# Kernel optimization log

Hardware: AMD Instinct MI355X
Metric: run time of the kernel (lower is better)

The kernel has to match this reference:

```python
import jax, jax.numpy as jnp
import numpy as np
import math

WIN = 2
TOPK = 3
GH, GW = 4, 4  # gabor splatting grid == upsampled window size


def _window_partition(img, ws):
    # img: (B, C, H, W) -> (B, num_windows, ws*ws, C)
    B, C, H, W = img.shape
    x = img.transpose(0, 2, 3, 1)  # B,H,W,C
    x = x.reshape(B, H // ws, ws, W // ws, ws, C)
    x = x.transpose(0, 1, 3, 2, 4, 5).reshape(B, -1, ws * ws, C)
    return x


def _gabor_map(theta, sigma, lam, psi, gamma):
    # build num 4x4 Gabor kernels from per-component params -> (num, GH, GW)
    cy = jnp.arange(GH, dtype=jnp.float32) - (GH - 1) / 2.0
    cx = jnp.arange(GW, dtype=jnp.float32) - (GW - 1) / 2.0
    yy, xx = jnp.meshgrid(cy, cx, indexing='ij')  # (GH, GW)
    th = theta[:, None, None] * (2.0 * jnp.pi)
    xp = xx[None] * jnp.cos(th) + yy[None] * jnp.sin(th)
    yp = -xx[None] * jnp.sin(th) + yy[None] * jnp.cos(th)
    sig = sigma[:, None, None] + 0.5  # keep positive
    lmb = lam[:, None, None] + 0.5
    gam = gamma[:, None, None]
    env = jnp.exp(-(xp ** 2 + (gam ** 2) * yp ** 2) / (2.0 * sig ** 2))
    carrier = jnp.cos(2.0 * jnp.pi * xp / lmb + psi[:, None, None])
    return env * carrier  # (num, GH, GW)


def setup_inputs() -> dict:
    key = jax.random.key(0)
    ks = jax.random.split(key, 8)
    B, Nt, Ns, C = 64, 64, 4096, 256
    return {
        'z': jax.random.normal(ks[0], (B, Nt, C), dtype=jnp.float32),
        'x': jax.random.normal(ks[1], (B, Ns, C), dtype=jnp.float32),
        'gabor_theta': jax.random.uniform(ks[2], (16,), dtype=jnp.float32),
        'gabor_sigma': jax.random.uniform(ks[3], (16,), dtype=jnp.float32),
        'gabor_lam': jax.random.uniform(ks[4], (16,), dtype=jnp.float32),
        'gabor_psi': jax.random.uniform(ks[5], (16,), dtype=jnp.float32),
        'gabor_gamma': jax.random.uniform(ks[6], (16,), dtype=jnp.float32),
        'gabor_weight': jax.random.normal(ks[7], (16,), dtype=jnp.float32),
    }


def reference(z, x, gabor_theta, gabor_sigma, gabor_lam, gabor_psi,
              gabor_gamma, gabor_weight):
    B, Nt, C = z.shape
    ht = int(math.isqrt(Nt))
    _, Ns, _ = x.shape
    hs = int(math.isqrt(Ns))

    z_img = z.transpose(0, 2, 1).reshape(B, C, ht, ht)
    z_max = z_img.max(axis=(2, 3))  # AdaptiveMaxPool2d((1,1)) -> (B, C)

    x_img = x.transpose(0, 2, 1).reshape(B, C, hs, hs)
    x_windows = _window_partition(x_img, WIN)

    # grouped 1x1 xcorr == per-pixel dot product with template vector
    response = jnp.einsum('bchw,bc->bhw', x_img, z_max)[:, None]  # (B,1,hs,hs)
    r_windows = _window_partition(response, WIN)
    win_mean = r_windows.mean(axis=2)[..., 0]  # (B, nW)

    _, idx = jax.lax.top_k(win_mean, TOPK)  # (B, TOPK)
    x_sel = jnp.take_along_axis(x_windows, idx[:, :, None, None], axis=1)
    x_win = x_sel.reshape(B, TOPK, WIN, WIN, C).transpose(0, 1, 4, 2, 3)
    x_win = x_win.reshape(B * TOPK, C, WIN, WIN)

    x_up = jax.image.resize(x_win, (B * TOPK, C, GH, GW), method='bilinear')

    g = _gabor_map(gabor_theta, gabor_sigma, gabor_lam, gabor_psi, gabor_gamma)
    gmap = jnp.einsum('k,khw->hw', gabor_weight, g)  # (GH, GW)
    splat = x_up * gmap  # gabor splatting as multiplicative spatial modulation

    res = (splat + x_up).reshape(B, TOPK, C, GH * GW)
    res = res.transpose(0, 1, 3, 2).reshape(B, TOPK * GH * GW, C)
    return res
```

## Files before the change

### kernel.cpp

```cpp
#include <hip/hip_runtime.h>
#include <math.h>

#define TWO_PI 6.28318530717958647692f

typedef float vfloat4 __attribute__((ext_vector_type(4)));


__global__ void k_zmax(const float* __restrict__ z, float* __restrict__ zmax) {
    int b = blockIdx.x;
    int c = threadIdx.x;
    const float* zp = z + (size_t)b * 64 * 256 + c;
    float m = -INFINITY;
#pragma unroll
    for (int n = 0; n < 64; ++n) m = fmaxf(m, zp[n * 256]);
    zmax[b * 256 + c] = m;
}

__global__ void k_wmean(const float* __restrict__ x, const float* __restrict__ zmax,
                        float* __restrict__ wmean) {
    int blk  = blockIdx.x;
    int b    = blk >> 5;
    int wh   = blk & 31;
    int wave = threadIdx.x >> 6;
    int lane = threadIdx.x & 63;
    int g    = lane >> 4;
    int q    = lane & 15;

    const vfloat4* zm4 = (const vfloat4*)(zmax + b * 256);
    vfloat4 zm0 = zm4[q];
    vfloat4 zm1 = zm4[q + 16];
    vfloat4 zm2 = zm4[q + 32];
    vfloat4 zm3 = zm4[q + 48];

    const vfloat4* xb = (const vfloat4*)(x + (size_t)b * 4096 * 256);
    int trow = (2 * wh + (g >> 1)) * 64;
    float* wout = wmean + b * 1024 + wh * 32;

#pragma unroll
    for (int p = 0; p < 8; ++p) {
        int ww  = p * 4 + wave;
        int tok = trow + 2 * ww + (g & 1);
        const vfloat4* tp = xb + (size_t)tok * 64;
        vfloat4 v0 = __builtin_nontemporal_load(tp + q);
        vfloat4 v1 = __builtin_nontemporal_load(tp + q + 16);
        vfloat4 v2 = __builtin_nontemporal_load(tp + q + 32);
        vfloat4 v3 = __builtin_nontemporal_load(tp + q + 48);
        float d = v0.x * zm0.x + v0.y * zm0.y + v0.z * zm0.z + v0.w * zm0.w
                + v1.x * zm1.x + v1.y * zm1.y + v1.z * zm1.z + v1.w * zm1.w
                + v2.x * zm2.x + v2.y * zm2.y + v2.z * zm2.z + v2.w * zm2.w
                + v3.x * zm3.x + v3.y * zm3.y + v3.z * zm3.z + v3.w * zm3.w;
        d += __shfl_xor(d, 1, 64);
        d += __shfl_xor(d, 2, 64);
        d += __shfl_xor(d, 4, 64);
        d += __shfl_xor(d, 8, 64);
        d += __shfl_xor(d, 16, 64);
        d += __shfl_xor(d, 32, 64);
        if (lane == 0) wout[ww] = d * 0.25f;
    }
}

__global__ void k_out(const float* __restrict__ x, const float* __restrict__ wmean_g,
                      const float* __restrict__ theta, const float* __restrict__ sigma,
                      const float* __restrict__ lam,   const float* __restrict__ psi,
                      const float* __restrict__ gamma, const float* __restrict__ wgt,
                      float* __restrict__ out) {
    __shared__ float wmean[1024];
    __shared__ float rv[256];
    __shared__ int   ri[256];
    __shared__ float Xs[4 * 256];
    __shared__ float gm[16];
    __shared__ int   widx_s;

    int b = blockIdx.x / 3;
    int k = blockIdx.x % 3;
    int tid  = threadIdx.x;
    int tok  = tid >> 6;
    int lane = tid & 63;

    if (tid < 16) {
        int p = tid;
        float yy = (float)(p >> 2) - 1.5f;
        float xx = (float)(p & 3) - 1.5f;
        float acc = 0.0f;
        for (int kk = 0; kk < 16; ++kk) {
            float th = theta[kk] * TWO_PI;
            float sn, cs;
            sincosf(th, &sn, &cs);
            float xp = xx * cs + yy * sn;
            float yp = -xx * sn + yy * cs;
            float sig = sigma[kk] + 0.5f;
            float lmb = lam[kk] + 0.5f;
            float gam = gamma[kk];
            float env = expf(-(xp * xp + gam * gam * yp * yp) / (2.0f * sig * sig));
            float car = cosf(TWO_PI * xp / lmb + psi[kk]);
            acc += wgt[kk] * env * car;
        }
        gm[p] = 1.0f + acc;
    }

    for (int w = tid; w < 1024; w += 256) wmean[w] = wmean_g[b * 1024 + w];
    __syncthreads();

    for (int kk = 0; kk <= k; ++kk) {
        float bv = -INFINITY;
        int   bi = 1 << 30;
        for (int w = tid; w < 1024; w += 256) {
            float v = wmean[w];
            if (v > bv || (v == bv && w < bi)) { bv = v; bi = w; }
        }
        rv[tid] = bv; ri[tid] = bi;
        __syncthreads();
        for (int s = 128; s > 0; s >>= 1) {
            if (tid < s) {
                float v2 = rv[tid + s]; int i2 = ri[tid + s];
                if (v2 > rv[tid] || (v2 == rv[tid] && i2 < ri[tid])) { rv[tid] = v2; ri[tid] = i2; }
            }
            __syncthreads();
        }
        if (tid == 0) {
            widx_s = ri[0];
            wmean[ri[0]] = -INFINITY;
        }
        __syncthreads();
    }

    int widx = widx_s;
    int h0 = (widx >> 5) << 1;
    int w0 = (widx & 31) << 1;
    int token_id = (h0 + (tok >> 1)) * 64 + w0 + (tok & 1);
    float4 v = ((const float4*)(x + ((size_t)b * 4096 + token_id) * 256))[lane];
    ((float4*)Xs)[tok * 64 + lane] = v;
    __syncthreads();

    const float WT[4] = {1.0f, 0.75f, 0.25f, 0.0f};
    float4 x00 = ((const float4*)Xs)[0 * 64 + lane];
    float4 x01 = ((const float4*)Xs)[1 * 64 + lane];
    float4 x10 = ((const float4*)Xs)[2 * 64 + lane];
    float4 x11 = ((const float4*)Xs)[3 * 64 + lane];
    float4* ob = (float4*)(out + ((size_t)b * 48 + k * 16) * 256);
#pragma unroll
    for (int it = 0; it < 4; ++it) {
        int p  = it * 4 + (tid >> 6);
        int gy = p >> 2, gx = p & 3;
        float wy0 = WT[gy], wy1 = 1.0f - wy0;
        float wx0 = WT[gx], wx1 = 1.0f - wx0;
        float g = gm[p];
        float4 r;
        r.x = g * (wy0 * (wx0 * x00.x + wx1 * x01.x) + wy1 * (wx0 * x10.x + wx1 * x11.x));
        r.y = g * (wy0 * (wx0 * x00.y + wx1 * x01.y) + wy1 * (wx0 * x10.y + wx1 * x11.y));
        r.z = g * (wy0 * (wx0 * x00.z + wx1 * x01.z) + wy1 * (wx0 * x10.z + wx1 * x11.z));
        r.w = g * (wy0 * (wx0 * x00.w + wx1 * x01.w) + wy1 * (wx0 * x10.w + wx1 * x11.w));
        ob[(size_t)p * 64 + lane] = r;
    }
}

extern "C" void kernel_launch(void* const* d_in, const int* in_sizes, int n_in,
                              void* d_out, int out_size, void* d_ws, size_t ws_size,
                              hipStream_t stream) {
    const float* z     = (const float*)d_in[0];
    const float* x     = (const float*)d_in[1];
    const float* theta = (const float*)d_in[2];
    const float* sigma = (const float*)d_in[3];
    const float* lam   = (const float*)d_in[4];
    const float* psi   = (const float*)d_in[5];
    const float* gamma = (const float*)d_in[6];
    const float* wgt   = (const float*)d_in[7];
    float* out = (float*)d_out;

    float* ws    = (float*)d_ws;
    float* zmax  = ws;
    float* wmean = ws + 16384;

    k_zmax<<<64, 256, 0, stream>>>(z, zmax);
    k_wmean<<<2048, 256, 0, stream>>>(x, zmax, wmean);
    k_out<<<192, 256, 0, stream>>>(x, wmean, theta, sigma, lam, psi, gamma, wgt, out);
}
```

Baseline: 361.3 us.

## Fuse z max-pool into window-mean kernel and sum window tokens before dot

Removes the separate z max-pool kernel: each window-mean block now recomputes the per-batch channel max of z into shared memory before its main loop. The dot product is also restructured so each lane holds 4 channels, adds the four window tokens first, and then does a single 4-wide dot with z_max. This cuts one launch and the global round trip of z_max, and lowers the multiply count. In exchange z is re-read redundantly by 32 blocks per batch and each block gains a barrier, and the changed summation order can shift near-tied window means, which could alter the top-k pick.

```diff
diff --git a/kernel.cpp b/kernel.cpp
--- a/kernel.cpp
+++ b/kernel.cpp
@@ -6,49 +6,41 @@
 typedef float vfloat4 __attribute__((ext_vector_type(4)));
 
 
-__global__ void k_zmax(const float* __restrict__ z, float* __restrict__ zmax) {
-    int b = blockIdx.x;
-    int c = threadIdx.x;
-    const float* zp = z + (size_t)b * 64 * 256 + c;
-    float m = -INFINITY;
+__global__ void k_wmean(const float* __restrict__ z, const float* __restrict__ x,
+                        float* __restrict__ wmean) {
+    __shared__ float zs[256];
+    int blk = blockIdx.x;
+    int b   = blk >> 5;
+    int wh  = blk & 31;
+    int tid = threadIdx.x;
+
+    {
+        const float* zp = z + (size_t)b * 64 * 256 + tid;
+        float m = -INFINITY;
 #pragma unroll
-    for (int n = 0; n < 64; ++n) m = fmaxf(m, zp[n * 256]);
-    zmax[b * 256 + c] = m;
-}
+        for (int n = 0; n < 64; ++n) m = fmaxf(m, zp[n * 256]);
+        zs[tid] = m;
+    }
+    __syncthreads();
 
-__global__ void k_wmean(const float* __restrict__ x, const float* __restrict__ zmax,
-                        float* __restrict__ wmean) {
-    int blk  = blockIdx.x;
-    int b    = blk >> 5;
-    int wh   = blk & 31;
-    int wave = threadIdx.x >> 6;
-    int lane = threadIdx.x & 63;
-    int g    = lane >> 4;
-    int q    = lane & 15;
-
-    const vfloat4* zm4 = (const vfloat4*)(zmax + b * 256);
-    vfloat4 zm0 = zm4[q];
-    vfloat4 zm1 = zm4[q + 16];
-    vfloat4 zm2 = zm4[q + 32];
-    vfloat4 zm3 = zm4[q + 48];
+    int wave = tid >> 6;
+    int lane = tid & 63;
+    vfloat4 zm = ((const vfloat4*)zs)[lane];
 
     const vfloat4* xb = (const vfloat4*)(x + (size_t)b * 4096 * 256);
-    int trow = (2 * wh + (g >> 1)) * 64;
+    size_t rbase = (size_t)(2 * wh) * 64 * 64;
     float* wout = wmean + b * 1024 + wh * 32;
 
 #pragma unroll
     for (int p = 0; p < 8; ++p) {
-        int ww  = p * 4 + wave;
-        int tok = trow + 2 * ww + (g & 1);
-        const vfloat4* tp = xb + (size_t)tok * 64;
-        vfloat4 v0 = __builtin_nontemporal_load(tp + q);
-        vfloat4 v1 = __builtin_nontemporal_load(tp + q + 16);
-        vfloat4 v2 = __builtin_nontemporal_load(tp + q + 32);
-        vfloat4 v3 = __builtin_nontemporal_load(tp + q + 48);
-        float d = v0.x * zm0.x + v0.y * zm0.y + v0.z * zm0.z + v0.w * zm0.w
-                + v1.x * zm1.x + v1.y * zm1.y + v1.z * zm1.z + v1.w * zm1.w
-                + v2.x * zm2.x + v2.y * zm2.y + v2.z * zm2.z + v2.w * zm2.w
-                + v3.x * zm3.x + v3.y * zm3.y + v3.z * zm3.z + v3.w * zm3.w;
+        int ww = p * 4 + wave;
+        const vfloat4* t00 = xb + rbase + (size_t)(2 * ww) * 64;
+        vfloat4 v00 = __builtin_nontemporal_load(t00 + lane);
+        vfloat4 v01 = __builtin_nontemporal_load(t00 + 64 + lane);
+        vfloat4 v10 = __builtin_nontemporal_load(t00 + 4096 + lane);
+        vfloat4 v11 = __builtin_nontemporal_load(t00 + 4096 + 64 + lane);
+        vfloat4 s = v00 + v01 + v10 + v11;
+        float d = s.x * zm.x + s.y * zm.y + s.z * zm.z + s.w * zm.w;
         d += __shfl_xor(d, 1, 64);
         d += __shfl_xor(d, 2, 64);
         d += __shfl_xor(d, 4, 64);
@@ -167,11 +159,8 @@
     const float* wgt   = (const float*)d_in[7];
     float* out = (float*)d_out;
 
-    float* ws    = (float*)d_ws;
-    float* zmax  = ws;
-    float* wmean = ws + 16384;
+    float* wmean = (float*)d_ws;
 
-    k_zmax<<<64, 256, 0, stream>>>(z, zmax);
-    k_wmean<<<2048, 256, 0, stream>>>(x, zmax, wmean);
+    k_wmean<<<2048, 256, 0, stream>>>(z, x, wmean);
     k_out<<<192, 256, 0, stream>>>(x, wmean, theta, sigma, lam, psi, gamma, wgt, out);
 }
```

New measurement: 368.3 us. About the same (+1.9%).
